# Performance work log

Measured on AMD Instinct MI355X. Metric: run time of the kernel, lower is better.

Reference implementation:

```python
import jax, jax.numpy as jnp
import numpy as np

D_MODEL = 1024
N_HEADS = 16
HEAD_DIM = D_MODEL // N_HEADS
SCALE = HEAD_DIM ** -0.5
MIN_VAL = jnp.finfo(jnp.float32).min


def setup_inputs() -> dict:
    key = jax.random.key(0)
    ks = jax.random.split(key, 7)
    B, T = 1, 2048
    s = D_MODEL ** -0.5
    return {
        "x": jax.random.normal(ks[0], (B, T, D_MODEL), dtype=jnp.float32),
        "Wq": jax.random.normal(ks[1], (D_MODEL, D_MODEL), dtype=jnp.float32) * s,
        "Wk1": jax.random.normal(ks[2], (D_MODEL, D_MODEL), dtype=jnp.float32) * s,
        "Wk2": jax.random.normal(ks[3], (D_MODEL, D_MODEL), dtype=jnp.float32) * s,
        "Wv": jax.random.normal(ks[4], (D_MODEL, D_MODEL), dtype=jnp.float32) * s,
        "Wo": jax.random.normal(ks[5], (D_MODEL, D_MODEL), dtype=jnp.float32) * s,
        "lambda_logit": jnp.zeros((N_HEADS,), dtype=jnp.float32),  # logit(0.5)=0
    }


def _split_heads(y):
    B, T, _ = y.shape
    return y.reshape(B, T, N_HEADS, HEAD_DIM).transpose(0, 2, 1, 3)  # [B,H,T,hd]


def reference(x, Wq, Wk1, Wk2, Wv, Wo, lambda_logit):
    B, T, _ = x.shape
    q = _split_heads(x @ Wq.T)
    k1 = _split_heads(x @ Wk1.T)
    k2 = _split_heads(x @ Wk2.T)
    v = _split_heads(x @ Wv.T)

    s1 = jnp.einsum("bhqd,bhkd->bhqk", q, k1) * SCALE
    s2 = jnp.einsum("bhqd,bhkd->bhqk", q, k2) * SCALE

    causal = jnp.arange(T)[None, :] <= jnp.arange(T)[:, None]  # [T,T] keep mask
    s1 = jnp.where(causal[None, None], s1, MIN_VAL)
    s2 = jnp.where(causal[None, None], s2, MIN_VAL)

    attn_exp = jax.nn.softmax(s1, axis=-1)
    attn_noise = jax.nn.softmax(s2, axis=-1)
    lam = jax.nn.sigmoid(lambda_logit)[None, :, None, None]
    attn = attn_exp - lam * attn_noise
    denom = jnp.maximum(jnp.sum(jnp.abs(attn), axis=-1, keepdims=True), 1e-6)
    attn = attn / denom

    out = jnp.einsum("bhqk,bhkd->bhqd", attn, v)
    out = out.transpose(0, 2, 1, 3).reshape(B, T, D_MODEL)
    return out @ Wo.T
```

## Files before the change

### kernel.cpp

```cpp
#include <hip/hip_runtime.h>

#define T_SEQ 2048
#define DM 1024
#define NH 16
#define HD 64
#define SC2 0.1803368801111731f
#define LS 80

typedef unsigned short u16;
typedef unsigned int u32;
typedef __attribute__((ext_vector_type(8))) short bf16x8;
typedef __attribute__((ext_vector_type(4))) float f32x4;

static __device__ __forceinline__ f32x4 mfma16(bf16x8 a, bf16x8 b, f32x4 c) {
    return __builtin_amdgcn_mfma_f32_16x16x32_bf16(a, b, c, 0, 0, 0);
}
static __device__ __forceinline__ float bf2f(u16 u) {
    union { u32 i; float f; } v; v.i = ((u32)u) << 16; return v.f;
}
static __device__ __forceinline__ u16 f2bf(float f) {
    union { float f; u32 i; } v; v.f = f;
    u32 x = v.i;
    x += 0x7FFFu + ((x >> 16) & 1u);
    return (u16)(x >> 16);
}
static __device__ __forceinline__ u16 f2bf_t(float f) {
    union { float f; u32 i; } v; v.f = f;
    return (u16)(v.i >> 16);
}
static __device__ __forceinline__ u32 pk2(float lo, float hi) {
    return (u32)f2bf(lo) | ((u32)f2bf(hi) << 16);
}
static __device__ __forceinline__ uint4 ld8(const void* src, size_t idx, int f) {
    if (f) return *(const uint4*)((const u16*)src + idx);
    const float* s = (const float*)src + idx;
    uint4 a = *(const uint4*)s;
    uint4 b = *(const uint4*)(s + 4);
    const float* af = (const float*)&a;
    const float* bf = (const float*)&b;
    uint4 r;
    r.x = pk2(af[0], af[1]); r.y = pk2(af[2], af[3]);
    r.z = pk2(bf[0], bf[1]); r.w = pk2(bf[2], bf[3]);
    return r;
}
static __device__ __forceinline__ float qsum16(float v) {
#pragma unroll
    for (int o = 1; o < 16; o <<= 1) v += __shfl_xor(v, o, 64);
    return v;
}
static __device__ __forceinline__ float ex2(float x) {
    return __builtin_amdgcn_exp2f(x);
}

static __device__ __forceinline__ void gl16(const u16* g, u16* l) {
    __builtin_amdgcn_global_load_lds(
        (const __attribute__((address_space(1))) void*)g,
        (__attribute__((address_space(3))) void*)l,
        16, 0, 0);
}

template <int NISS>
static __device__ __forceinline__ void stage_async(const u16* src, size_t row0,
                                                   size_t lds_, size_t col0,
                                                   u16* dst, int tid) {
#pragma unroll
    for (int it = 0; it < NISS; it++) {
        int r = it * 32 + (tid >> 3);
        int cg = (tid & 7) ^ (r & 7);
        gl16(&src[(row0 + r) * lds_ + col0 + cg * 8], &dst[(it * 256 + tid) * 8]);
    }
}
template <int NISS>
static __device__ __forceinline__ void stage_sync(const void* src, size_t row0,
                                                  size_t lds_, size_t col0,
                                                  u16* dst, int tid, int f) {
#pragma unroll
    for (int it = 0; it < NISS; it++) {
        int r = it * 32 + (tid >> 3);
        int cg = (tid & 7) ^ (r & 7);
        *(uint4*)(&dst[(it * 256 + tid) * 8]) =
            ld8(src, (row0 + r) * lds_ + col0 + cg * 8, f);
    }
}
static __device__ __forceinline__ bf16x8 frag(const u16* buf, int R, int co) {
    return *(const bf16x8*)(&buf[R * 64 + co]);
}

__global__ void detect_lam(const u16* __restrict__ x, const void* __restrict__ lamsrc,
                           int* __restrict__ flag, float* __restrict__ lamf) {
    __shared__ int tot;
    if (threadIdx.x == 0) tot = 0;
    __syncthreads();
    int c = 0;
    for (int i = threadIdx.x; i < 1024; i += 256) {
        u16 v = x[2 * i];
        int e = (v >> 7) & 0xFF;
        c += (e >= 110 && e <= 140) ? 1 : 0;
    }
    atomicAdd(&tot, c);
    __syncthreads();
    const int f = (tot >= 512) ? 1 : 0;
    if (threadIdx.x == 0) *flag = f;
    if (threadIdx.x < NH) {
        float v = f ? bf2f(((const u16*)lamsrc)[threadIdx.x])
                    : ((const float*)lamsrc)[threadIdx.x];
        lamf[threadIdx.x] = 1.0f / (1.0f + __expf(-v));
    }
}

__global__ __launch_bounds__(256) void qkv_gemm(
    const void* __restrict__ xs, const void* __restrict__ wq,
    const void* __restrict__ wk1, const void* __restrict__ wk2,
    const void* __restrict__ wv, const int* __restrict__ flag,
    u16* __restrict__ qd, u16* __restrict__ k1d, u16* __restrict__ k2d,
    u16* __restrict__ vtd) {
    __shared__ __align__(16) u16 As[2][128 * 64];
    __shared__ __align__(16) u16 Bs[2][64 * 64];

    const int f = *flag;
    const int w = blockIdx.x >> 4;
    const int n0 = (blockIdx.x & 15) * 64;
    const int m0 = blockIdx.y * 128;
    const void* Bpv = (w == 0) ? wq : (w == 1) ? wk1 : (w == 2) ? wk2 : wv;
    const u16* xb = (const u16*)xs;
    const u16* Bb = (const u16*)Bpv;

    const int tid = threadIdx.x;
    const int lane = tid & 63, wave = tid >> 6;
    const int lr = lane & 15, quad = lane >> 4;
    const int wm = (wave >> 1) * 64, wn = (wave & 1) * 32;
    const int sw = lr & 7;

    f32x4 acc[4][2];
#pragma unroll
    for (int i = 0; i < 4; i++)
#pragma unroll
        for (int j = 0; j < 2; j++) acc[i][j] = (f32x4){0.f, 0.f, 0.f, 0.f};

    if (f) {
        stage_async<4>(xb, m0, DM, 0, As[0], tid);
        stage_async<2>(Bb, n0, DM, 0, Bs[0], tid);
    }
    for (int k0 = 0; k0 < DM; k0 += 64) {
        const int cur = (k0 >> 6) & 1;
        __syncthreads();
        if (f) {
            if (k0 + 64 < DM) {
                stage_async<4>(xb, m0, DM, k0 + 64, As[cur ^ 1], tid);
                stage_async<2>(Bb, n0, DM, k0 + 64, Bs[cur ^ 1], tid);
            }
        } else {
            stage_sync<4>(xs, m0, DM, k0, As[cur], tid, 0);
            stage_sync<2>(Bpv, n0, DM, k0, Bs[cur], tid, 0);
            __syncthreads();
        }
#pragma unroll
        for (int kk = 0; kk < 2; kk++) {
            const int co = ((kk * 4 + quad) ^ sw) * 8;
            bf16x8 af[4], bfr[2];
#pragma unroll
            for (int i = 0; i < 4; i++) af[i] = frag(As[cur], wm + i * 16 + lr, co);
#pragma unroll
            for (int j = 0; j < 2; j++) bfr[j] = frag(Bs[cur], wn + j * 16 + lr, co);
#pragma unroll
            for (int i = 0; i < 4; i++)
#pragma unroll
                for (int j = 0; j < 2; j++) acc[i][j] = mfma16(af[i], bfr[j], acc[i][j]);
        }
    }

#pragma unroll
    for (int i = 0; i < 4; i++)
#pragma unroll
        for (int j = 0; j < 2; j++)
#pragma unroll
            for (int r = 0; r < 4; r++) {
                int t = m0 + wm + i * 16 + quad * 4 + r;
                int o = n0 + wn + j * 16 + lr;
                float val = acc[i][j][r];
                if (w == 0) val *= SC2;
                u16 vbits = f2bf(val);
                int hh = o >> 6, d0 = o & 63;
                if (w == 3)
                    vtd[((size_t)hh * HD + d0) * T_SEQ + t] = vbits;
                else
                    ((w == 0) ? qd : (w == 1) ? k1d : k2d)[((size_t)hh * T_SEQ + t) * HD + d0] = vbits;
            }
}

#define ATTN_MAP()                                            \
    const int b = blockIdx.x;                                 \
    const int par = b >> 9;                                   \
    const int rem = b & 511;                                  \
    const int h = rem & 15;                                   \
    const int bi = rem >> 4;                                  \
    const int qt = (bi < 16) ? bi : 47 - bi;                  \
    const int t0 = qt * 64;                                   \
    const int tid = threadIdx.x;                              \
    const int lane = tid & 63, wave = tid >> 6;               \
    const int lr = lane & 15, quad = lane >> 4;               \
    const int wm = wave * 16;                                 \
    const int sw = lr & 7;

__global__ __launch_bounds__(256) void attn_a(
    const u16* __restrict__ qg, const u16* __restrict__ k1g,
    const u16* __restrict__ k2g, float* __restrict__ zp) {
    __shared__ __align__(16) u16 k1s[64 * 64];
    __shared__ __align__(16) u16 k2s[64 * 64];
    ATTN_MAP();

    const u16* qh = qg + (size_t)h * T_SEQ * HD;
    const u16* k1h = k1g + (size_t)h * T_SEQ * HD;
    const u16* k2h = k2g + (size_t)h * T_SEQ * HD;

    bf16x8 aq[2];
#pragma unroll
    for (int kk = 0; kk < 2; kk++)
        aq[kk] = *(const bf16x8*)(&qh[(size_t)(t0 + wm + lr) * HD + kk * 32 + quad * 8]);

    float z1a[4] = {0.f, 0.f, 0.f, 0.f}, z2a[4] = {0.f, 0.f, 0.f, 0.f};

    for (int kt = par; kt <= qt; kt += 2) {
        __syncthreads();
        stage_async<2>(k1h, (size_t)kt * 64, HD, 0, k1s, tid);
        stage_async<2>(k2h, (size_t)kt * 64, HD, 0, k2s, tid);
        __syncthreads();

        f32x4 sa[4], sb[4];
#pragma unroll
        for (int j = 0; j < 4; j++) { sa[j] = (f32x4){0.f,0.f,0.f,0.f}; sb[j] = (f32x4){0.f,0.f,0.f,0.f}; }
#pragma unroll
        for (int kk = 0; kk < 2; kk++) {
            const int co = ((kk * 4 + quad) ^ sw) * 8;
#pragma unroll
            for (int j = 0; j < 4; j++) {
                sa[j] = mfma16(aq[kk], frag(k1s, j * 16 + lr, co), sa[j]);
                sb[j] = mfma16(aq[kk], frag(k2s, j * 16 + lr, co), sb[j]);
            }
        }

        if (kt < qt) {
#pragma unroll
            for (int r = 0; r < 4; r++)
#pragma unroll
                for (int j = 0; j < 4; j++) {
                    z1a[r] += ex2(sa[j][r]);
                    z2a[r] += ex2(sb[j][r]);
                }
        } else {
#pragma unroll
            for (int r = 0; r < 4; r++) {
                const int grow = t0 + wm + quad * 4 + r;
#pragma unroll
                for (int j = 0; j < 4; j++) {
                    int gcol = kt * 64 + j * 16 + lr;
                    if (gcol <= grow) {
                        z1a[r] += ex2(sa[j][r]);
                        z2a[r] += ex2(sb[j][r]);
                    }
                }
            }
        }
    }

#pragma unroll
    for (int r = 0; r < 4; r++) {
        float s1 = qsum16(z1a[r]);
        float s2 = qsum16(z2a[r]);
        if (lr == 0) {
            int row = t0 + wm + quad * 4 + r;
            zp[((size_t)(par * 2 + 0) * NH + h) * T_SEQ + row] = s1;
            zp[((size_t)(par * 2 + 1) * NH + h) * T_SEQ + row] = s2;
        }
    }
}

__global__ __launch_bounds__(256) void attn_b(
    const u16* __restrict__ qg, const u16* __restrict__ k1g,
    const u16* __restrict__ k2g, const u16* __restrict__ vtg,
    const float* __restrict__ zp, const float* __restrict__ lamf,
    float* __restrict__ dpart, u16* __restrict__ opart) {
    __shared__ __align__(16) u16 k1s[64 * 64];
    __shared__ __align__(16) u16 k2s[64 * 64];
    __shared__ __align__(16) u16 vs[64 * 64];
    __shared__ __align__(16) u16 ps[4][16 * LS];
    ATTN_MAP();
    const float lam = lamf[h];

    const u16* qh = qg + (size_t)h * T_SEQ * HD;
    const u16* k1h = k1g + (size_t)h * T_SEQ * HD;
    const u16* k2h = k2g + (size_t)h * T_SEQ * HD;
    const u16* vh = vtg + (size_t)h * HD * T_SEQ;

    bf16x8 aq[2];
#pragma unroll
    for (int kk = 0; kk < 2; kk++)
        aq[kk] = *(const bf16x8*)(&qh[(size_t)(t0 + wm + lr) * HD + kk * 32 + quad * 8]);

    float z1i[4], z2i[4];
#pragma unroll
    for (int r = 0; r < 4; r++) {
        int row = t0 + wm + quad * 4 + r;
        float z1 = zp[((size_t)0 * NH + h) * T_SEQ + row] + zp[((size_t)2 * NH + h) * T_SEQ + row];
        float z2 = zp[((size_t)1 * NH + h) * T_SEQ + row] + zp[((size_t)3 * NH + h) * T_SEQ + row];
        z1i[r] = 1.f / z1;
        z2i[r] = lam / z2;
    }

    f32x4 oac[4];
#pragma unroll
    for (int j = 0; j < 4; j++) oac[j] = (f32x4){0.f, 0.f, 0.f, 0.f};
    float dacc[4] = {0.f, 0.f, 0.f, 0.f};

    for (int kt = par; kt <= qt; kt += 2) {
        __syncthreads();
        stage_async<2>(k1h, (size_t)kt * 64, HD, 0, k1s, tid);
        stage_async<2>(k2h, (size_t)kt * 64, HD, 0, k2s, tid);
        stage_async<2>(vh, 0, T_SEQ, (size_t)kt * 64, vs, tid);
        __syncthreads();

        f32x4 sa[4], sb[4];
#pragma unroll
        for (int j = 0; j < 4; j++) { sa[j] = (f32x4){0.f,0.f,0.f,0.f}; sb[j] = (f32x4){0.f,0.f,0.f,0.f}; }
#pragma unroll
        for (int kk = 0; kk < 2; kk++) {
            const int co = ((kk * 4 + quad) ^ sw) * 8;
#pragma unroll
            for (int j = 0; j < 4; j++) {
                sa[j] = mfma16(aq[kk], frag(k1s, j * 16 + lr, co), sa[j]);
                sb[j] = mfma16(aq[kk], frag(k2s, j * 16 + lr, co), sb[j]);
            }
        }

        if (kt < qt) {
#pragma unroll
            for (int r = 0; r < 4; r++)
#pragma unroll
                for (int j = 0; j < 4; j++) {
                    float p = ex2(sa[j][r]) * z1i[r] - ex2(sb[j][r]) * z2i[r];
                    dacc[r] += fabsf(p);
                    ps[wave][(quad * 4 + r) * LS + j * 16 + lr] = f2bf_t(p);
                }
        } else {
#pragma unroll
            for (int r = 0; r < 4; r++) {
                const int grow = t0 + wm + quad * 4 + r;
#pragma unroll
                for (int j = 0; j < 4; j++) {
                    int gcol = kt * 64 + j * 16 + lr;
                    float p = 0.f;
                    if (gcol <= grow)
                        p = ex2(sa[j][r]) * z1i[r] - ex2(sb[j][r]) * z2i[r];
                    dacc[r] += fabsf(p);
                    ps[wave][(quad * 4 + r) * LS + j * 16 + lr] = f2bf_t(p);
                }
            }
        }

#pragma unroll
        for (int kk = 0; kk < 2; kk++) {
            bf16x8 pa = *(const bf16x8*)(&ps[wave][lr * LS + kk * 32 + quad * 8]);
            const int co = ((kk * 4 + quad) ^ sw) * 8;
#pragma unroll
            for (int j = 0; j < 4; j++)
                oac[j] = mfma16(pa, frag(vs, j * 16 + lr, co), oac[j]);
        }
    }

#pragma unroll
    for (int r = 0; r < 4; r++) {
        float ds = qsum16(dacc[r]);
        if (lr == 0) {
            int row = t0 + wm + quad * 4 + r;
            dpart[((size_t)par * NH + h) * T_SEQ + row] = ds;
        }
    }
#pragma unroll
    for (int j = 0; j < 4; j++)
#pragma unroll
        for (int r = 0; r < 4; r++) {
            int row = t0 + wm + quad * 4 + r;
            opart[(size_t)par * T_SEQ * DM + (size_t)row * DM + h * HD + j * 16 + lr] =
                f2bf(oac[j][r]);
        }
}

__global__ __launch_bounds__(256) void normalize_o(
    const u16* __restrict__ opart, const float* __restrict__ dpart,
    u16* __restrict__ ao) {
    int g = blockIdx.x * 256 + threadIdx.x;
    int t = g >> 7;
    int cc = g & 127;
    int d0 = cc * 8;
    int h = d0 >> 6;
    float dsum = dpart[(size_t)h * T_SEQ + t] + dpart[(size_t)(NH + h) * T_SEQ + t];
    float rs = 1.f / fmaxf(dsum, 1e-6f);
    uint4 a = *(const uint4*)(&opart[(size_t)t * DM + d0]);
    uint4 bqq = *(const uint4*)(&opart[(size_t)T_SEQ * DM + (size_t)t * DM + d0]);
    const u32* au = (const u32*)&a;
    const u32* bu = (const u32*)&bqq;
    uint4 out;
    u32* ou = (u32*)&out;
#pragma unroll
    for (int i = 0; i < 4; i++) {
        float lo = (bf2f((u16)(au[i] & 0xFFFF)) + bf2f((u16)(bu[i] & 0xFFFF))) * rs;
        float hi = (bf2f((u16)(au[i] >> 16)) + bf2f((u16)(bu[i] >> 16))) * rs;
        ou[i] = pk2(lo, hi);
    }
    *(uint4*)(&ao[(size_t)t * DM + d0]) = out;
}

__global__ __launch_bounds__(256) void out_gemm(
    const u16* __restrict__ ab, const void* __restrict__ wo,
    const int* __restrict__ flag, void* __restrict__ outp) {
    __shared__ __align__(16) u16 As[2][128 * 64];
    __shared__ __align__(16) u16 Bs[2][64 * 64];

    const int f = *flag;
    const int n0 = blockIdx.x * 64;
    const int m0 = blockIdx.y * 128;
    const u16* wb = (const u16*)wo;
    const int tid = threadIdx.x;
    const int lane = tid & 63, wave = tid >> 6;
    const int lr = lane & 15, quad = lane >> 4;
    const int wm = (wave >> 1) * 64, wn = (wave & 1) * 32;
    const int sw = lr & 7;

    f32x4 acc[4][2];
#pragma unroll
    for (int i = 0; i < 4; i++)
#pragma unroll
        for (int j = 0; j < 2; j++) acc[i][j] = (f32x4){0.f, 0.f, 0.f, 0.f};

    if (f) {
        stage_async<4>(ab, m0, DM, 0, As[0], tid);
        stage_async<2>(wb, n0, DM, 0, Bs[0], tid);
    }
    for (int k0 = 0; k0 < DM; k0 += 64) {
        const int cur = (k0 >> 6) & 1;
        __syncthreads();
        if (f) {
            if (k0 + 64 < DM) {
                stage_async<4>(ab, m0, DM, k0 + 64, As[cur ^ 1], tid);
                stage_async<2>(wb, n0, DM, k0 + 64, Bs[cur ^ 1], tid);
            }
        } else {
            stage_sync<4>(ab, m0, DM, k0, As[cur], tid, 1);
            stage_sync<2>(wo, n0, DM, k0, Bs[cur], tid, 0);
            __syncthreads();
        }
#pragma unroll
        for (int kk = 0; kk < 2; kk++) {
            const int co = ((kk * 4 + quad) ^ sw) * 8;
            bf16x8 af[4], bfr[2];
#pragma unroll
            for (int i = 0; i < 4; i++) af[i] = frag(As[cur], wm + i * 16 + lr, co);
#pragma unroll
            for (int j = 0; j < 2; j++) bfr[j] = frag(Bs[cur], wn + j * 16 + lr, co);
#pragma unroll
            for (int i = 0; i < 4; i++)
#pragma unroll
                for (int j = 0; j < 2; j++) acc[i][j] = mfma16(af[i], bfr[j], acc[i][j]);
        }
    }

#pragma unroll
    for (int i = 0; i < 4; i++)
#pragma unroll
        for (int j = 0; j < 2; j++)
#pragma unroll
            for (int r = 0; r < 4; r++) {
                int t = m0 + wm + i * 16 + quad * 4 + r;
                int o = n0 + wn + j * 16 + lr;
                float val = acc[i][j][r];
                if (f)
                    ((u16*)outp)[(size_t)t * DM + o] = f2bf(val);
                else
                    ((float*)outp)[(size_t)t * DM + o] = val;
            }
}

extern "C" void kernel_launch(void* const* d_in, const int* in_sizes, int n_in,
                              void* d_out, int out_size, void* d_ws, size_t ws_size,
                              hipStream_t stream) {
    char* ws = (char*)d_ws;
    int* flag = (int*)(ws + 0);
    float* lamf = (float*)(ws + 256);
    float* zp    = (float*)(ws + ((size_t)1 << 20));
    float* dpart = (float*)(ws + ((size_t)2 << 20));
    u16* qd  = (u16*)(ws + ((size_t)16 << 20));
    u16* k1d = (u16*)(ws + ((size_t)20 << 20));
    u16* k2d = (u16*)(ws + ((size_t)24 << 20));
    u16* vtd = (u16*)(ws + ((size_t)28 << 20));
    u16* ao  = (u16*)(ws + ((size_t)32 << 20));
    u16* opart = (u16*)(ws + ((size_t)36 << 20));

    detect_lam<<<1, 256, 0, stream>>>((const u16*)d_in[0], d_in[6], flag, lamf);
    qkv_gemm<<<dim3(64, 16), 256, 0, stream>>>(d_in[0], d_in[1], d_in[2], d_in[3],
                                               d_in[4], flag, qd, k1d, k2d, vtd);
    attn_a<<<dim3(1024), 256, 0, stream>>>(qd, k1d, k2d, zp);
    attn_b<<<dim3(1024), 256, 0, stream>>>(qd, k1d, k2d, vtd, zp, lamf, dpart, opart);
    normalize_o<<<dim3(1024), 256, 0, stream>>>(opart, dpart, ao);
    out_gemm<<<dim3(16, 16), 256, 0, stream>>>(ao, d_in[5], flag, d_out);
}
```

Before: 225.0 us.

## Drop LDS staging and load MFMA fragments directly from global memory

New measurement: 536.6 us. +138.4%, slower.

```diff
diff --git a/kernel.cpp b/kernel.cpp
--- a/kernel.cpp
+++ b/kernel.cpp
@@ -43,6 +43,9 @@
     r.z = pk2(bf[0], bf[1]); r.w = pk2(bf[2], bf[3]);
     return r;
 }
+static __device__ __forceinline__ bf16x8 as_bf(uint4 v) {
+    union { uint4 u; bf16x8 b; } c; c.u = v; return c.b;
+}
 static __device__ __forceinline__ float qsum16(float v) {
 #pragma unroll
     for (int o = 1; o < 16; o <<= 1) v += __shfl_xor(v, o, 64);
@@ -50,40 +53,6 @@
 }
 static __device__ __forceinline__ float ex2(float x) {
     return __builtin_amdgcn_exp2f(x);
-}
-
-static __device__ __forceinline__ void gl16(const u16* g, u16* l) {
-    __builtin_amdgcn_global_load_lds(
-        (const __attribute__((address_space(1))) void*)g,
-        (__attribute__((address_space(3))) void*)l,
-        16, 0, 0);
-}
-
-template <int NISS>
-static __device__ __forceinline__ void stage_async(const u16* src, size_t row0,
-                                                   size_t lds_, size_t col0,
-                                                   u16* dst, int tid) {
-#pragma unroll
-    for (int it = 0; it < NISS; it++) {
-        int r = it * 32 + (tid >> 3);
-        int cg = (tid & 7) ^ (r & 7);
-        gl16(&src[(row0 + r) * lds_ + col0 + cg * 8], &dst[(it * 256 + tid) * 8]);
-    }
-}
-template <int NISS>
-static __device__ __forceinline__ void stage_sync(const void* src, size_t row0,
-                                                  size_t lds_, size_t col0,
-                                                  u16* dst, int tid, int f) {
-#pragma unroll
-    for (int it = 0; it < NISS; it++) {
-        int r = it * 32 + (tid >> 3);
-        int cg = (tid & 7) ^ (r & 7);
-        *(uint4*)(&dst[(it * 256 + tid) * 8]) =
-            ld8(src, (row0 + r) * lds_ + col0 + cg * 8, f);
-    }
-}
-static __device__ __forceinline__ bf16x8 frag(const u16* buf, int R, int co) {
-    return *(const bf16x8*)(&buf[R * 64 + co]);
 }
 
 __global__ void detect_lam(const u16* __restrict__ x, const void* __restrict__ lamsrc,
@@ -114,22 +83,16 @@
     const void* __restrict__ wv, const int* __restrict__ flag,
     u16* __restrict__ qd, u16* __restrict__ k1d, u16* __restrict__ k2d,
     u16* __restrict__ vtd) {
-    __shared__ __align__(16) u16 As[2][128 * 64];
-    __shared__ __align__(16) u16 Bs[2][64 * 64];
-
     const int f = *flag;
     const int w = blockIdx.x >> 4;
     const int n0 = (blockIdx.x & 15) * 64;
     const int m0 = blockIdx.y * 128;
     const void* Bpv = (w == 0) ? wq : (w == 1) ? wk1 : (w == 2) ? wk2 : wv;
-    const u16* xb = (const u16*)xs;
-    const u16* Bb = (const u16*)Bpv;
 
     const int tid = threadIdx.x;
     const int lane = tid & 63, wave = tid >> 6;
     const int lr = lane & 15, quad = lane >> 4;
     const int wm = (wave >> 1) * 64, wn = (wave & 1) * 32;
-    const int sw = lr & 7;
 
     f32x4 acc[4][2];
 #pragma unroll
@@ -137,36 +100,23 @@
 #pragma unroll
         for (int j = 0; j < 2; j++) acc[i][j] = (f32x4){0.f, 0.f, 0.f, 0.f};
 
-    if (f) {
-        stage_async<4>(xb, m0, DM, 0, As[0], tid);
-        stage_async<2>(Bb, n0, DM, 0, Bs[0], tid);
-    }
-    for (int k0 = 0; k0 < DM; k0 += 64) {
-        const int cur = (k0 >> 6) & 1;
-        __syncthreads();
-        if (f) {
-            if (k0 + 64 < DM) {
-                stage_async<4>(xb, m0, DM, k0 + 64, As[cur ^ 1], tid);
-                stage_async<2>(Bb, n0, DM, k0 + 64, Bs[cur ^ 1], tid);
-            }
-        } else {
-            stage_sync<4>(xs, m0, DM, k0, As[cur], tid, 0);
-            stage_sync<2>(Bpv, n0, DM, k0, Bs[cur], tid, 0);
-            __syncthreads();
-        }
-#pragma unroll
-        for (int kk = 0; kk < 2; kk++) {
-            const int co = ((kk * 4 + quad) ^ sw) * 8;
-            bf16x8 af[4], bfr[2];
-#pragma unroll
-            for (int i = 0; i < 4; i++) af[i] = frag(As[cur], wm + i * 16 + lr, co);
-#pragma unroll
-            for (int j = 0; j < 2; j++) bfr[j] = frag(Bs[cur], wn + j * 16 + lr, co);
-#pragma unroll
-            for (int i = 0; i < 4; i++)
-#pragma unroll
-                for (int j = 0; j < 2; j++) acc[i][j] = mfma16(af[i], bfr[j], acc[i][j]);
-        }
+    size_t abase[4], bbase[2];
+#pragma unroll
+    for (int i = 0; i < 4; i++) abase[i] = (size_t)(m0 + wm + i * 16 + lr) * DM + quad * 8;
+#pragma unroll
+    for (int j = 0; j < 2; j++) bbase[j] = (size_t)(n0 + wn + j * 16 + lr) * DM + quad * 8;
+
+#pragma unroll 2
+    for (int ks = 0; ks < DM; ks += 32) {
+        bf16x8 af[4], bfr[2];
+#pragma unroll
+        for (int i = 0; i < 4; i++) af[i] = as_bf(ld8(xs, abase[i] + ks, f));
+#pragma unroll
+        for (int j = 0; j < 2; j++) bfr[j] = as_bf(ld8(Bpv, bbase[j] + ks, f));
+#pragma unroll
+        for (int i = 0; i < 4; i++)
+#pragma unroll
+            for (int j = 0; j < 2; j++) acc[i][j] = mfma16(af[i], bfr[j], acc[i][j]);
     }
 
 #pragma unroll
@@ -199,14 +149,11 @@
     const int tid = threadIdx.x;                              \
     const int lane = tid & 63, wave = tid >> 6;               \
     const int lr = lane & 15, quad = lane >> 4;               \
-    const int wm = wave * 16;                                 \
-    const int sw = lr & 7;
+    const int wm = wave * 16;
 
 __global__ __launch_bounds__(256) void attn_a(
     const u16* __restrict__ qg, const u16* __restrict__ k1g,
     const u16* __restrict__ k2g, float* __restrict__ zp) {
-    __shared__ __align__(16) u16 k1s[64 * 64];
-    __shared__ __align__(16) u16 k2s[64 * 64];
     ATTN_MAP();
 
     const u16* qh = qg + (size_t)h * T_SEQ * HD;
@@ -221,21 +168,18 @@
     float z1a[4] = {0.f, 0.f, 0.f, 0.f}, z2a[4] = {0.f, 0.f, 0.f, 0.f};
 
     for (int kt = par; kt <= qt; kt += 2) {
-        __syncthreads();
-        stage_async<2>(k1h, (size_t)kt * 64, HD, 0, k1s, tid);
-        stage_async<2>(k2h, (size_t)kt * 64, HD, 0, k2s, tid);
-        __syncthreads();
-
         f32x4 sa[4], sb[4];
 #pragma unroll
         for (int j = 0; j < 4; j++) { sa[j] = (f32x4){0.f,0.f,0.f,0.f}; sb[j] = (f32x4){0.f,0.f,0.f,0.f}; }
 #pragma unroll
         for (int kk = 0; kk < 2; kk++) {
-            const int co = ((kk * 4 + quad) ^ sw) * 8;
 #pragma unroll
             for (int j = 0; j < 4; j++) {
-                sa[j] = mfma16(aq[kk], frag(k1s, j * 16 + lr, co), sa[j]);
-                sb[j] = mfma16(aq[kk], frag(k2s, j * 16 + lr, co), sb[j]);
+                size_t off = (size_t)(kt * 64 + j * 16 + lr) * HD + kk * 32 + quad * 8;
+                bf16x8 b1 = *(const bf16x8*)(&k1h[off]);
+                bf16x8 b2 = *(const bf16x8*)(&k2h[off]);
+                sa[j] = mfma16(aq[kk], b1, sa[j]);
+                sb[j] = mfma16(aq[kk], b2, sb[j]);
             }
         }
 
@@ -280,9 +224,6 @@
     const u16* __restrict__ k2g, const u16* __restrict__ vtg,
     const float* __restrict__ zp, const float* __restrict__ lamf,
     float* __restrict__ dpart, u16* __restrict__ opart) {
-    __shared__ __align__(16) u16 k1s[64 * 64];
-    __shared__ __align__(16) u16 k2s[64 * 64];
-    __shared__ __align__(16) u16 vs[64 * 64];
     __shared__ __align__(16) u16 ps[4][16 * LS];
     ATTN_MAP();
     const float lam = lamf[h];
@@ -313,22 +254,18 @@
     float dacc[4] = {0.f, 0.f, 0.f, 0.f};
 
     for (int kt = par; kt <= qt; kt += 2) {
-        __syncthreads();
-        stage_async<2>(k1h, (size_t)kt * 64, HD, 0, k1s, tid);
-        stage_async<2>(k2h, (size_t)kt * 64, HD, 0, k2s, tid);
-        stage_async<2>(vh, 0, T_SEQ, (size_t)kt * 64, vs, tid);
-        __syncthreads();
-
         f32x4 sa[4], sb[4];
 #pragma unroll
         for (int j = 0; j < 4; j++) { sa[j] = (f32x4){0.f,0.f,0.f,0.f}; sb[j] = (f32x4){0.f,0.f,0.f,0.f}; }
 #pragma unroll
         for (int kk = 0; kk < 2; kk++) {
-            const int co = ((kk * 4 + quad) ^ sw) * 8;
 #pragma unroll
             for (int j = 0; j < 4; j++) {
-                sa[j] = mfma16(aq[kk], frag(k1s, j * 16 + lr, co), sa[j]);
-                sb[j] = mfma16(aq[kk], frag(k2s, j * 16 + lr, co), sb[j]);
+                size_t off = (size_t)(kt * 64 + j * 16 + lr) * HD + kk * 32 + quad * 8;
+                bf16x8 b1 = *(const bf16x8*)(&k1h[off]);
+                bf16x8 b2 = *(const bf16x8*)(&k2h[off]);
+                sa[j] = mfma16(aq[kk], b1, sa[j]);
+                sb[j] = mfma16(aq[kk], b2, sb[j]);
             }
         }
 
@@ -360,10 +297,12 @@
 #pragma unroll
         for (int kk = 0; kk < 2; kk++) {
             bf16x8 pa = *(const bf16x8*)(&ps[wave][lr * LS + kk * 32 + quad * 8]);
-            const int co = ((kk * 4 + quad) ^ sw) * 8;
-#pragma unroll
-            for (int j = 0; j < 4; j++)
-                oac[j] = mfma16(pa, frag(vs, j * 16 + lr, co), oac[j]);
+#pragma unroll
+            for (int j = 0; j < 4; j++) {
+                bf16x8 vb = *(const bf16x8*)(&vh[(size_t)(j * 16 + lr) * T_SEQ +
+                                                 kt * 64 + kk * 32 + quad * 8]);
+                oac[j] = mfma16(pa, vb, oac[j]);
+            }
         }
     }
 
@@ -413,18 +352,13 @@
 __global__ __launch_bounds__(256) void out_gemm(
     const u16* __restrict__ ab, const void* __restrict__ wo,
     const int* __restrict__ flag, void* __restrict__ outp) {
-    __shared__ __align__(16) u16 As[2][128 * 64];
-    __shared__ __align__(16) u16 Bs[2][64 * 64];
-
     const int f = *flag;
     const int n0 = blockIdx.x * 64;
     const int m0 = blockIdx.y * 128;
-    const u16* wb = (const u16*)wo;
     const int tid = threadIdx.x;
     const int lane = tid & 63, wave = tid >> 6;
     const int lr = lane & 15, quad = lane >> 4;
     const int wm = (wave >> 1) * 64, wn = (wave & 1) * 32;
-    const int sw = lr & 7;
 
     f32x4 acc[4][2];
 #pragma unroll
@@ -432,36 +366,23 @@
 #pragma unroll
         for (int j = 0; j < 2; j++) acc[i][j] = (f32x4){0.f, 0.f, 0.f, 0.f};
 
-    if (f) {
-        stage_async<4>(ab, m0, DM, 0, As[0], tid);
-        stage_async<2>(wb, n0, DM, 0, Bs[0], tid);
-    }
-    for (int k0 = 0; k0 < DM; k0 += 64) {
-        const int cur = (k0 >> 6) & 1;
-        __syncthreads();
-        if (f) {
-            if (k0 + 64 < DM) {
-                stage_async<4>(ab, m0, DM, k0 + 64, As[cur ^ 1], tid);
-                stage_async<2>(wb, n0, DM, k0 + 64, Bs[cur ^ 1], tid);
-            }
-        } else {
-            stage_sync<4>(ab, m0, DM, k0, As[cur], tid, 1);
-            stage_sync<2>(wo, n0, DM, k0, Bs[cur], tid, 0);
-            __syncthreads();
-        }
-#pragma unroll
-        for (int kk = 0; kk < 2; kk++) {
-            const int co = ((kk * 4 + quad) ^ sw) * 8;
-            bf16x8 af[4], bfr[2];
-#pragma unroll
-            for (int i = 0; i < 4; i++) af[i] = frag(As[cur], wm + i * 16 + lr, co);
-#pragma unroll
-            for (int j = 0; j < 2; j++) bfr[j] = frag(Bs[cur], wn + j * 16 + lr, co);
-#pragma unroll
-            for (int i = 0; i < 4; i++)
-#pragma unroll
-                for (int j = 0; j < 2; j++) acc[i][j] = mfma16(af[i], bfr[j], acc[i][j]);
-        }
+    size_t abase[4], bbase[2];
+#pragma unroll
+    for (int i = 0; i < 4; i++) abase[i] = (size_t)(m0 + wm + i * 16 + lr) * DM + quad * 8;
+#pragma unroll
+    for (int j = 0; j < 2; j++) bbase[j] = (size_t)(n0 + wn + j * 16 + lr) * DM + quad * 8;
+
+#pragma unroll 2
+    for (int ks = 0; ks < DM; ks += 32) {
+        bf16x8 af[4], bfr[2];
+#pragma unroll
+        for (int i = 0; i < 4; i++) af[i] = *(const bf16x8*)(&ab[abase[i] + ks]);
+#pragma unroll
+        for (int j = 0; j < 2; j++) bfr[j] = as_bf(ld8(wo, bbase[j] + ks, f));
+#pragma unroll
+        for (int i = 0; i < 4; i++)
+#pragma unroll
+            for (int j = 0; j < 2; j++) acc[i][j] = mfma16(af[i], bfr[j], acc[i][j]);
     }
 
 #pragma unroll
```
